# Performance work log

Measured on AMD Instinct MI355X. Metric: run time of the kernel, lower is better.

Reference implementation:

```python
import jax, jax.numpy as jnp
import numpy as np

B, H, M, K = 256, 1024, 20, 20  # batch, hidden, max_ingr, pairing top_k (must be equal: M==K)
VOCAB, INGR_V = 32000, 5000


def setup_inputs() -> dict:
    key = jax.random.key(0)
    ks = jax.random.split(key, 24)
    s = 0.02
    inp = {
        "input_ids": jax.random.randint(ks[0], (1, B), 0, VOCAB),
        "hidden": jax.random.normal(ks[1], (1, B, H), jnp.float32),
        "encoder_outputs": jax.random.normal(ks[2], (M, B, 2 * H), jnp.float32),
        "input_tensor": jax.random.randint(ks[3], (B, M), 0, INGR_V),
        "pairing_ids": jax.random.randint(ks[4], (INGR_V, K), 0, INGR_V),
        # parameters
        "emb_dec": jax.random.normal(ks[5], (VOCAB, H), jnp.float32) * s,
        "enc_emb": jax.random.normal(ks[6], (INGR_V, 2 * H), jnp.float32) * s,
        "Wq_i": jax.random.normal(ks[7], (H, H), jnp.float32) * s,
        "Wk_i": jax.random.normal(ks[8], (2 * H, H), jnp.float32) * s,
        "wa_i": jax.random.normal(ks[9], (H,), jnp.float32) * s,
        "Wq_p": jax.random.normal(ks[10], (H, H), jnp.float32) * s,
        "Wk_p": jax.random.normal(ks[11], (2 * H, H), jnp.float32) * s,
        "wa_p": jax.random.normal(ks[12], (H,), jnp.float32) * s,
        "ba_p": jax.random.normal(ks[13], (), jnp.float32) * s,
        "W_lin": jax.random.normal(ks[14], (3 * H, 2 * H), jnp.float32) * s,
        "b_lin": jnp.zeros((2 * H,), jnp.float32),
        "W_ih": jax.random.normal(ks[15], (3 * H, 2 * H), jnp.float32) * s,
        "W_hh": jax.random.normal(ks[16], (3 * H, H), jnp.float32) * s,
        "b_ih": jnp.zeros((3 * H,), jnp.float32),
        "b_hh": jnp.zeros((3 * H,), jnp.float32),
        "W_out": jax.random.normal(ks[17], (H, VOCAB), jnp.float32) * s,
        "b_out": jnp.zeros((VOCAB,), jnp.float32),
    }
    return inp


def reference(input_ids, hidden, encoder_outputs, input_tensor, pairing_ids,
              emb_dec, enc_emb, Wq_i, Wk_i, wa_i, Wq_p, Wk_p, wa_p, ba_p,
              W_lin, b_lin, W_ih, W_hh, b_ih, b_hh, W_out, b_out):
    h = hidden[0]                              # (B, H)
    emb = jnp.take(emb_dec, input_ids[0], axis=0)  # (B, H)

    # ---- IngrAtt (additive attention over ingredients) ----
    # torch code does a raw .view(B, M, 2H) on a (M, B, 2H) tensor -> plain reshape
    enc = encoder_outputs.reshape(B, M, 2 * H)
    query = h @ Wq_i                           # (B, H)
    key = enc @ Wk_i                           # (B, M, H)
    scores_i = jnp.tanh(query[:, None, :] + key) @ wa_i  # (B, M)
    aw = jax.nn.softmax(scores_i, axis=-1)     # (B, M)

    # ---- retrieval: pick most-attended ingredient, gather its top-k pairings ----
    ingr_arg = jnp.argmax(aw, axis=1)                          # (B,)
    ingr_id = input_tensor[jnp.arange(B), ingr_arg]            # (B,)
    comp_ids = jnp.take(pairing_ids, ingr_id, axis=0)          # (B, K)
    comp_emb = jnp.take(enc_emb, comp_ids, axis=0)             # (B, K, 2H)

    # ---- PairingAtt ----
    q_p = h @ Wq_p                             # (B, H)
    k_p = comp_emb @ Wk_p                      # (B, K, H)
    s_p = jnp.tanh(q_p[:, None, :] + k_p) @ wa_p + ba_p  # (B, K)
    a_p = jax.nn.softmax(s_p, axis=-1)
    attn_scores = a_p * s_p                    # (B, K) softmax-weighted raw scores
    attn_app = jnp.einsum('bk,bkd->bd', attn_scores, comp_emb)  # (B, 2H)

    out_pair = jnp.concatenate([emb, attn_app], axis=-1)  # (B, 3H)
    x = out_pair @ W_lin + b_lin                           # (B, 2H) -> GRU input

    # ---- single GRU step (torch gate ordering r,z,n) ----
    gi = x @ W_ih.T + b_ih
    gh = h @ W_hh.T + b_hh
    i_r, i_z, i_n = jnp.split(gi, 3, axis=-1)
    h_r, h_z, h_n = jnp.split(gh, 3, axis=-1)
    r = jax.nn.sigmoid(i_r + h_r)
    z = jax.nn.sigmoid(i_z + h_z)
    n = jnp.tanh(i_n + r * h_n)
    h_new = (1.0 - z) * n + z * h              # (B, H)

    logits = h_new @ W_out + b_out             # (B, VOCAB)
    return logits
```

## Files before the change

kernel.cpp:

```cpp
#include <hip/hip_runtime.h>
#include <cstdio>


using f32x4   = __attribute__((ext_vector_type(4))) float;
using bf16x8  = __attribute__((ext_vector_type(8))) short;
using ushort8 = __attribute__((ext_vector_type(8))) unsigned short;

__device__ __forceinline__ unsigned short f2bf(float x) {
    unsigned u = __builtin_bit_cast(unsigned, x);
    u += 0x7fffu + ((u >> 16) & 1u);
    return (unsigned short)(u >> 16);
}
__device__ __forceinline__ float bf2f(unsigned short u) {
    return __builtin_bit_cast(float, ((unsigned)u) << 16);
}

__device__ __forceinline__ void gload16(const void* g, void* l) {
    auto gp = (const __attribute__((address_space(1))) void*)g;
    auto lp = (__attribute__((address_space(3))) void*)l;
    __builtin_amdgcn_global_load_lds(gp, lp, 16, 0, 0);
}

__device__ __forceinline__ void transpose_body(
    const float* __restrict__ in, unsigned short* __restrict__ out,
    int R, int C, int r0, int c0)
{
    __shared__ float t[32][129];
    const int tid = threadIdx.x;
    const int lr = tid >> 3;
    const int cc = (tid & 7) * 4;
    #pragma unroll
    for (int i = 0; i < 4; ++i) {
        int r = lr + 32 * i;
        float4 v = *(const float4*)(in + (size_t)(r0 + r) * C + c0 + cc);
        t[cc + 0][r] = v.x; t[cc + 1][r] = v.y;
        t[cc + 2][r] = v.z; t[cc + 3][r] = v.w;
    }
    __syncthreads();
    const int rc = (tid & 15) * 8;
    #pragma unroll
    for (int p = 0; p < 2; ++p) {
        int c = (tid >> 4) + 16 * p;
        const float* src = &t[c][rc];
        ushort8 o;
        #pragma unroll
        for (int j = 0; j < 8; ++j) o[j] = f2bf(src[j]);
        *(ushort8*)(out + (size_t)(c0 + c) * R + r0 + rc) = o;
    }
}

__global__ __launch_bounds__(256) void prep1_kernel(
    const float* __restrict__ hidden, const float* __restrict__ enc_out,
    const float* __restrict__ enc_emb,
    const float* __restrict__ Wq_i, const float* __restrict__ Wq_p,
    const float* __restrict__ Wk_i, const float* __restrict__ Wk_p,
    unsigned short* __restrict__ hb, unsigned short* __restrict__ encb,
    unsigned short* __restrict__ encembb,
    unsigned short* __restrict__ WqiT, unsigned short* __restrict__ WqpT,
    unsigned short* __restrict__ WkiT, unsigned short* __restrict__ WkpT)
{
    const int bid = blockIdx.x;
    if (bid < 20496) {
        int i = bid * 256 + threadIdx.x;
        const float* src; unsigned short* dst; int j;
        if (i < 65536)        { src = hidden;  dst = hb;      j = i; }
        else if (i < 2686976) { src = enc_out; dst = encb;    j = i - 65536; }
        else                  { src = enc_emb; dst = encembb; j = i - 2686976; }
        float4 v = ((const float4*)src)[j];
        ((ushort4*)dst)[j] = make_ushort4(f2bf(v.x), f2bf(v.y), f2bf(v.z), f2bf(v.w));
    } else if (bid < 21008) {
        int local = bid - 20496;
        int bz = local >> 8, rem = local & 255;
        transpose_body(bz ? Wq_p : Wq_i, bz ? WqpT : WqiT,
                       1024, 1024, (rem >> 5) * 128, (rem & 31) * 32);
    } else {
        int local = bid - 21008;
        int bz = local >> 9, rem = local & 511;
        transpose_body(bz ? Wk_p : Wk_i, bz ? WkpT : WkiT,
                       2048, 1024, (rem >> 5) * 128, (rem & 31) * 32);
    }
}

template<int OUTBF, bool HAS_BIAS>
__device__ __forceinline__ void gemm_core(
    const unsigned short* __restrict__ A, const unsigned short* __restrict__ Bt,
    const float* __restrict__ bias, void* __restrict__ Cout, int Ncols,
    int sA, int sB, int kLen, int m0, int n0,
    unsigned short* lA, unsigned short* lB)
{
    const int tid = threadIdx.x;
    const int lane = tid & 63, wave = tid >> 6;
    const int wr = wave >> 1, wc = wave & 1;
    const int srow = tid >> 3, schunk = tid & 7;
    const int lm = lane & 15, lk = (lane >> 4) * 8;

    f32x4 acc[4][4];
    #pragma unroll
    for (int m = 0; m < 4; ++m)
        #pragma unroll
        for (int n = 0; n < 4; ++n) { f32x4 z = {0.f,0.f,0.f,0.f}; acc[m][n] = z; }

    const unsigned short* Ag = A  + (size_t)(m0 + srow) * sA + schunk * 8;
    const unsigned short* Bg = Bt + (size_t)(n0 + srow) * sB + schunk * 8;
    const int nt = kLen >> 6;

    char* lap = (char*)lA + tid * 16;
    char* lbp = (char*)lB + tid * 16;

    for (int t = 0; t < nt; ++t) {
        #pragma unroll
        for (int i = 0; i < 4; ++i) {
            gload16(Ag + (size_t)(32 * i) * sA + t * 64, lap + i * 4096);
            gload16(Bg + (size_t)(32 * i) * sB + t * 64, lbp + i * 4096);
        }
        __syncthreads();
        #pragma unroll
        for (int kk = 0; kk < 2; ++kk) {
            bf16x8 af[4], bv[4];
            #pragma unroll
            for (int m = 0; m < 4; ++m)
                af[m] = *(const bf16x8*)((const char*)lA +
                          (wr * 64 + m * 16 + lm) * 128 + (kk * 32 + lk) * 2);
            #pragma unroll
            for (int n = 0; n < 4; ++n)
                bv[n] = *(const bf16x8*)((const char*)lB +
                          (wc * 64 + n * 16 + lm) * 128 + (kk * 32 + lk) * 2);
            #pragma unroll
            for (int m = 0; m < 4; ++m)
                #pragma unroll
                for (int n = 0; n < 4; ++n)
                    acc[m][n] = __builtin_amdgcn_mfma_f32_16x16x32_bf16(
                        af[m], bv[n], acc[m][n], 0, 0, 0);
        }
        __syncthreads();
    }

    const int rbase = m0 + wr * 64 + (lane >> 4) * 4;
    const int cbase = n0 + wc * 64 + lm;
    #pragma unroll
    for (int m = 0; m < 4; ++m) {
        #pragma unroll
        for (int n = 0; n < 4; ++n) {
            int col = cbase + n * 16;
            float bvv = HAS_BIAS ? bias[col] : 0.0f;
            #pragma unroll
            for (int j = 0; j < 4; ++j) {
                int row = rbase + m * 16 + j;
                float v = acc[m][n][j] + bvv;
                if (OUTBF)
                    ((unsigned short*)Cout)[(size_t)row * Ncols + col] = f2bf(v);
                else
                    ((float*)Cout)[(size_t)row * Ncols + col] = v;
            }
        }
    }
}

#define GEMM_SHARED \
    __shared__ unsigned short lA[8192]; __shared__ unsigned short lB[8192];

__global__ __launch_bounds__(256) void gemm_dual_kernel(
    const unsigned short* A, const unsigned short* B0, const unsigned short* B1,
    float* P0, float* P1)
{
    GEMM_SHARED
    const int g = blockIdx.z >> 2, s = blockIdx.z & 3;
    const unsigned short* Bt = (g ? B1 : B0) + s * 256;
    float* C = (g ? P1 : P0) + (size_t)s * 262144;
    gemm_core<0,false>(A + s * 256, Bt, nullptr, C, 1024, 1024, 1024, 256,
                       blockIdx.y * 128, blockIdx.x * 128, lA, lB);
}

__global__ __launch_bounds__(256) void reduceq_kernel(
    const float* __restrict__ pqQ, const float* __restrict__ pqP,
    float* __restrict__ query, float* __restrict__ qp)
{
    int i = blockIdx.x * 256 + threadIdx.x;
    const float4* p; float4* o; int j;
    if (i < 65536) { p = (const float4*)pqQ; o = (float4*)query; j = i; }
    else           { p = (const float4*)pqP; o = (float4*)qp;    j = i - 65536; }
    float4 a = p[j], b = p[j + 65536], c = p[j + 131072], d = p[j + 196608];
    o[j] = make_float4(a.x + b.x + c.x + d.x, a.y + b.y + c.y + d.y,
                       a.z + b.z + c.z + d.z, a.w + b.w + c.w + d.w);
}

__global__ __launch_bounds__(256) void gemm24_kernel(
    const unsigned short* encembb, const unsigned short* encb,
    const unsigned short* WkpT, const unsigned short* WkiT,
    unsigned short* kpP, unsigned short* keyP, size_t pStride)
{
    GEMM_SHARED
    const int g = blockIdx.z >> 1, h = blockIdx.z & 1;
    const unsigned short* A  = (g ? encb : encembb) + h * 1024;
    const unsigned short* Bt = (g ? WkiT : WkpT)    + h * 1024;
    unsigned short* C = (g ? keyP : kpP) + (size_t)h * pStride;
    gemm_core<1,false>(A, Bt, nullptr, C, 1024, 2048, 2048, 1024,
                       blockIdx.y * 128, blockIdx.x * 128, lA, lB);
}

__global__ __launch_bounds__(256) void gemm5f_kernel(
    const unsigned short* __restrict__ A, const float* __restrict__ Wlin,
    float* __restrict__ P)
{
    __shared__ unsigned short lA[8192];
    __shared__ unsigned short lB[8192];
    const int tid = threadIdx.x;
    const int lane = tid & 63, wave = tid >> 6;
    const int wr = wave >> 1, wc = wave & 1;
    const int m0 = blockIdx.y * 128, n0 = blockIdx.x * 128;
    const int koff = blockIdx.z * 384;
    const int srow = tid >> 3, schunk = tid & 7;
    const int lm = lane & 15, lk = (lane >> 4) * 8;
    const int bcol = tid & 127, bkg = tid >> 7;
    const int bsw  = (bcol & 7) << 4;

    f32x4 acc[4][4];
    #pragma unroll
    for (int m = 0; m < 4; ++m)
        #pragma unroll
        for (int n = 0; n < 4; ++n) { f32x4 z = {0.f,0.f,0.f,0.f}; acc[m][n] = z; }

    const unsigned short* Ag = A + (size_t)(m0 + srow) * 3072 + koff + schunk * 8;
    char* lap = (char*)lA + tid * 16;

    for (int t = 0; t < 6; ++t) {
        #pragma unroll
        for (int i = 0; i < 4; ++i)
            gload16(Ag + (size_t)(32 * i) * 3072 + t * 64, lap + i * 4096);
        #pragma unroll
        for (int hh = 0; hh < 2; ++hh) {
            const int kbase = koff + t * 64 + bkg * 32 + hh * 16;
            ushort8 o0, o1;
            #pragma unroll
            for (int j = 0; j < 8; ++j)
                o0[j] = f2bf(Wlin[(size_t)(kbase + j) * 2048 + n0 + bcol]);
            #pragma unroll
            for (int j = 0; j < 8; ++j)
                o1[j] = f2bf(Wlin[(size_t)(kbase + 8 + j) * 2048 + n0 + bcol]);
            char* base = (char*)lB + bcol * 128;
            *(ushort8*)(base + ((bkg * 64 + hh * 32)      ^ bsw)) = o0;
            *(ushort8*)(base + ((bkg * 64 + hh * 32 + 16) ^ bsw)) = o1;
        }
        __syncthreads();
        #pragma unroll
        for (int kk = 0; kk < 2; ++kk) {
            bf16x8 af[4], bv[4];
            #pragma unroll
            for (int m = 0; m < 4; ++m)
                af[m] = *(const bf16x8*)((const char*)lA +
                          (wr * 64 + m * 16 + lm) * 128 + (kk * 32 + lk) * 2);
            #pragma unroll
            for (int n = 0; n < 4; ++n) {
                int rr = wc * 64 + n * 16 + lm;
                bv[n] = *(const bf16x8*)((const char*)lB +
                          rr * 128 + (((kk * 32 + lk) * 2) ^ ((rr & 7) << 4)));
            }
            #pragma unroll
            for (int m = 0; m < 4; ++m)
                #pragma unroll
                for (int n = 0; n < 4; ++n)
                    acc[m][n] = __builtin_amdgcn_mfma_f32_16x16x32_bf16(
                        af[m], bv[n], acc[m][n], 0, 0, 0);
        }
        __syncthreads();
    }

    float* C = P + (size_t)blockIdx.z * 524288;
    const int rbase = m0 + wr * 64 + (lane >> 4) * 4;
    const int cbase = n0 + wc * 64 + lm;
    #pragma unroll
    for (int m = 0; m < 4; ++m)
        #pragma unroll
        for (int n = 0; n < 4; ++n)
            #pragma unroll
            for (int j = 0; j < 4; ++j)
                C[(size_t)(rbase + m * 16 + j) * 2048 + cbase + n * 16] = acc[m][n][j];
}

__global__ __launch_bounds__(256) void gemm67f_kernel(
    const unsigned short* __restrict__ xb, const unsigned short* __restrict__ hb,
    const float* __restrict__ Wih, const float* __restrict__ Whh,
    float* __restrict__ pg)
{
    __shared__ unsigned short lA[8192];
    __shared__ unsigned short lB[8192];
    const int tid = threadIdx.x;
    const int lane = tid & 63, wave = tid >> 6;
    const int wr = wave >> 1, wc = wave & 1;
    const int g = blockIdx.z >> 2, s = blockIdx.z & 3;
    const unsigned short* A = g ? hb : xb;
    const float* Bf = g ? Whh : Wih;
    const int sA   = g ? 1024 : 2048;
    const int koff = g ? s * 256 : s * 512;
    const int nt   = g ? 4 : 8;
    const int m0 = blockIdx.y * 128, n0 = blockIdx.x * 128;
    const int srow = tid >> 3, schunk = tid & 7;
    const int lm = lane & 15, lk = (lane >> 4) * 8;
    const int bsw = (srow & 7) << 4;

    f32x4 acc[4][4];
    #pragma unroll
    for (int m = 0; m < 4; ++m)
        #pragma unroll
        for (int n = 0; n < 4; ++n) { f32x4 z = {0.f,0.f,0.f,0.f}; acc[m][n] = z; }

    const unsigned short* Ag = A  + (size_t)(m0 + srow) * sA + koff + schunk * 8;
    const float*          Bg = Bf + (size_t)(n0 + srow) * sA + koff + schunk * 8;
    char* lap = (char*)lA + tid * 16;

    for (int t = 0; t < nt; ++t) {
        #pragma unroll
        for (int i = 0; i < 4; ++i)
            gload16(Ag + (size_t)(32 * i) * sA + t * 64, lap + i * 4096);
        #pragma unroll
        for (int i = 0; i < 4; ++i) {
            const float* src = Bg + (size_t)(32 * i) * sA + t * 64;
            float4 v0 = *(const float4*)(src);
            float4 v1 = *(const float4*)(src + 4);
            ushort8 o;
            o[0] = f2bf(v0.x); o[1] = f2bf(v0.y); o[2] = f2bf(v0.z); o[3] = f2bf(v0.w);
            o[4] = f2bf(v1.x); o[5] = f2bf(v1.y); o[6] = f2bf(v1.z); o[7] = f2bf(v1.w);
            *(ushort8*)((char*)lB + (srow + 32 * i) * 128 + ((schunk * 16) ^ bsw)) = o;
        }
        __syncthreads();
        #pragma unroll
        for (int kk = 0; kk < 2; ++kk) {
            bf16x8 af[4], bv[4];
            #pragma unroll
            for (int m = 0; m < 4; ++m)
                af[m] = *(const bf16x8*)((const char*)lA +
                          (wr * 64 + m * 16 + lm) * 128 + (kk * 32 + lk) * 2);
            #pragma unroll
            for (int n = 0; n < 4; ++n) {
                int rr = wc * 64 + n * 16 + lm;
                bv[n] = *(const bf16x8*)((const char*)lB +
                          rr * 128 + (((kk * 32 + lk) * 2) ^ ((rr & 7) << 4)));
            }
            #pragma unroll
            for (int m = 0; m < 4; ++m)
                #pragma unroll
                for (int n = 0; n < 4; ++n)
                    acc[m][n] = __builtin_amdgcn_mfma_f32_16x16x32_bf16(
                        af[m], bv[n], acc[m][n], 0, 0, 0);
        }
        __syncthreads();
    }

    float* C = pg + (size_t)blockIdx.z * 786432;
    const int rbase = m0 + wr * 64 + (lane >> 4) * 4;
    const int cbase = n0 + wc * 64 + lm;
    #pragma unroll
    for (int m = 0; m < 4; ++m)
        #pragma unroll
        for (int n = 0; n < 4; ++n)
            #pragma unroll
            for (int j = 0; j < 4; ++j)
                C[(size_t)(rbase + m * 16 + j) * 3072 + cbase + n * 16] = acc[m][n][j];
}

__global__ __launch_bounds__(256) void gemm8_kernel(
    const unsigned short* __restrict__ A, const float* __restrict__ Wout,
    const float* __restrict__ bias, float* __restrict__ C)
{
    __shared__ unsigned short lA0[16384]; __shared__ unsigned short lA1[16384];
    __shared__ unsigned short lB0[4096];  __shared__ unsigned short lB1[4096];
    const int tid  = threadIdx.x;
    const int lane = tid & 63, wave = tid >> 6;
    const int n0 = blockIdx.x * 64;
    const int lm = lane & 15, lk = (lane >> 4) * 8;
    const int srow = tid >> 3, schunk = tid & 7;
    const int bcol = tid & 63, bkg = tid >> 6;
    const int bsw  = (bcol & 7) << 4;

    f32x4 acc[4][4];
    #pragma unroll
    for (int m = 0; m < 4; ++m)
        #pragma unroll
        for (int n = 0; n < 4; ++n) { f32x4 z = {0.f,0.f,0.f,0.f}; acc[m][n] = z; }

    const unsigned short* Ag = A + (size_t)srow * 1024 + schunk * 8;

    auto stageA = [&](unsigned short* la_, int t) {
        char* la = (char*)la_ + tid * 16;
        #pragma unroll
        for (int i = 0; i < 8; ++i)
            gload16(Ag + (size_t)(32 * i) * 1024 + t * 64, la + i * 4096);
    };
    float bv_[16];
    auto loadB = [&](int t) {
        const float* src = Wout + (size_t)(t * 64 + bkg * 16) * 32000 + n0 + bcol;
        #pragma unroll
        for (int j = 0; j < 16; ++j) bv_[j] = src[(size_t)j * 32000];
    };
    auto writeB = [&](unsigned short* lb_) {
        ushort8 o0, o1;
        #pragma unroll
        for (int j = 0; j < 8; ++j) { o0[j] = f2bf(bv_[j]); o1[j] = f2bf(bv_[j + 8]); }
        char* base = (char*)lb_ + bcol * 128;
        *(ushort8*)(base + ((bkg * 32)      ^ bsw)) = o0;
        *(ushort8*)(base + ((bkg * 32 + 16) ^ bsw)) = o1;
    };
    auto compute = [&](const unsigned short* la_, const unsigned short* lb_) {
        #pragma unroll
        for (int kk = 0; kk < 2; ++kk) {
            bf16x8 af[4], bv[4];
            #pragma unroll
            for (int m = 0; m < 4; ++m)
                af[m] = *(const bf16x8*)((const char*)la_ +
                          (wave * 64 + m * 16 + lm) * 128 + (kk * 32 + lk) * 2);
            #pragma unroll
            for (int n = 0; n < 4; ++n) {
                int rr = n * 16 + lm;
                bv[n] = *(const bf16x8*)((const char*)lb_ +
                          rr * 128 + (((kk * 32 + lk) * 2) ^ ((rr & 7) << 4)));
            }
            #pragma unroll
            for (int m = 0; m < 4; ++m)
                #pragma unroll
                for (int n = 0; n < 4; ++n)
                    acc[m][n] = __builtin_amdgcn_mfma_f32_16x16x32_bf16(
                        af[m], bv[n], acc[m][n], 0, 0, 0);
        }
    };

    stageA(lA0, 0); loadB(0); writeB(lB0);
    __syncthreads();
    const int nt = 16;
    for (int t = 0; t < nt; t += 2) {
        if (t + 1 < nt) { stageA(lA1, t + 1); loadB(t + 1); }
        compute(lA0, lB0);
        if (t + 1 < nt) writeB(lB1);
        __syncthreads();
        if (t + 1 < nt) {
            if (t + 2 < nt) { stageA(lA0, t + 2); loadB(t + 2); }
            compute(lA1, lB1);
            if (t + 2 < nt) writeB(lB0);
            __syncthreads();
        }
    }

    const int rbase = wave * 64 + (lane >> 4) * 4;
    const int cbase = n0 + lm;
    #pragma unroll
    for (int m = 0; m < 4; ++m) {
        #pragma unroll
        for (int n = 0; n < 4; ++n) {
            int col = cbase + n * 16;
            float bvv = bias[col];
            #pragma unroll
            for (int j = 0; j < 4; ++j)
                C[(size_t)(rbase + m * 16 + j) * 32000 + col] = acc[m][n][j] + bvv;
        }
    }
}

__global__ __launch_bounds__(256) void attn_scores2_kernel(
    const float* __restrict__ q, const unsigned short* __restrict__ kP,
    size_t kStride, const float* __restrict__ wa, float* __restrict__ scores)
{
    const int bm = blockIdx.x;
    const int b  = bm / 20;
    const int tid = threadIdx.x;
    float4 qv  = ((const float4*)(q + (size_t)b * 1024))[tid];
    ushort4 k0 = ((const ushort4*)(kP + (size_t)bm * 1024))[tid];
    ushort4 k1 = ((const ushort4*)(kP + kStride + (size_t)bm * 1024))[tid];
    float4 wv  = ((const float4*)wa)[tid];
    float p = tanhf(qv.x + bf2f(k0.x) + bf2f(k1.x)) * wv.x
            + tanhf(qv.y + bf2f(k0.y) + bf2f(k1.y)) * wv.y
            + tanhf(qv.z + bf2f(k0.z) + bf2f(k1.z)) * wv.z
            + tanhf(qv.w + bf2f(k0.w) + bf2f(k1.w)) * wv.w;
    #pragma unroll
    for (int off = 32; off > 0; off >>= 1) p += __shfl_down(p, off);
    __shared__ float sp[4];
    if ((tid & 63) == 0) sp[tid >> 6] = p;
    __syncthreads();
    if (tid == 0) scores[bm] = sp[0] + sp[1] + sp[2] + sp[3];
}

__device__ __forceinline__ int argmax_ing(
    const float* __restrict__ sc_i, const int* __restrict__ input_tensor, int b)
{
    float best = sc_i[b * 20]; int bi = 0;
    #pragma unroll
    for (int m = 1; m < 20; ++m) {
        float v = sc_i[b * 20 + m];
        if (v > best) { best = v; bi = m; }
    }
    return input_tensor[b * 20 + bi];
}

__global__ __launch_bounds__(256) void attn_scores_gather2_kernel(
    const float* __restrict__ q, const unsigned short* __restrict__ kP,
    size_t kStride, const float* __restrict__ wa, const float* __restrict__ ba,
    const float* __restrict__ sc_i, const int* __restrict__ input_tensor,
    const int* __restrict__ pairing_ids, float* __restrict__ scores)
{
    const int bm = blockIdx.x;
    const int b  = bm / 20;
    const int kk = bm - b * 20;
    const int tid = threadIdx.x;
    const int ing = argmax_ing(sc_i, input_tensor, b);
    const int cid = pairing_ids[ing * 20 + kk];
    float4 qv  = ((const float4*)(q + (size_t)b * 1024))[tid];
    ushort4 k0 = ((const ushort4*)(kP + (size_t)cid * 1024))[tid];
    ushort4 k1 = ((const ushort4*)(kP + kStride + (size_t)cid * 1024))[tid];
    float4 wv  = ((const float4*)wa)[tid];
    float p = tanhf(qv.x + bf2f(k0.x) + bf2f(k1.x)) * wv.x
            + tanhf(qv.y + bf2f(k0.y) + bf2f(k1.y)) * wv.y
            + tanhf(qv.z + bf2f(k0.z) + bf2f(k1.z)) * wv.z
            + tanhf(qv.w + bf2f(k0.w) + bf2f(k1.w)) * wv.w;
    #pragma unroll
    for (int off = 32; off > 0; off >>= 1) p += __shfl_down(p, off);
    __shared__ float sp[4];
    if ((tid & 63) == 0) sp[tid >> 6] = p;
    __syncthreads();
    if (tid == 0) scores[bm] = sp[0] + sp[1] + sp[2] + sp[3] + ba[0];
}

__global__ __launch_bounds__(256) void out_pair_kernel(
    const float* __restrict__ s_p, const float* __restrict__ enc_emb,
    const float* __restrict__ sc_i, const int* __restrict__ input_tensor,
    const int* __restrict__ pairing_ids,
    const float* __restrict__ emb_dec, const int* __restrict__ input_ids,
    unsigned short* __restrict__ out_pairb)
{
    const int b = blockIdx.x / 6, seg = blockIdx.x % 6;
    const int tid = threadIdx.x;
    const int d = seg * 512 + tid * 2;
    ushort2 o;
    if (seg < 2) {
        float2 v = *(const float2*)(emb_dec + (size_t)input_ids[b] * 1024 + d);
        o.x = f2bf(v.x); o.y = f2bf(v.y);
    } else {
        const int ing = argmax_ing(sc_i, input_tensor, b);
        __shared__ float s_raw[20];
        if (tid < 20) s_raw[tid] = s_p[b * 20 + tid];
        __syncthreads();
        float mx = -1e30f;
        #pragma unroll
        for (int m = 0; m < 20; ++m) mx = fmaxf(mx, s_raw[m]);
        float den = 0.f; float w[20];
        #pragma unroll
        for (int m = 0; m < 20; ++m) { w[m] = expf(s_raw[m] - mx); den += w[m]; }
        const float inv = 1.f / den;
        const int dd = d - 1024;
        float a0 = 0.f, a1 = 0.f;
        #pragma unroll
        for (int k = 0; k < 20; ++k) {
            const int cid = pairing_ids[ing * 20 + k];
            float2 v = *(const float2*)(enc_emb + (size_t)cid * 2048 + dd);
            float a = w[k] * inv * s_raw[k];
            a0 += a * v.x; a1 += a * v.y;
        }
        o.x = f2bf(a0); o.y = f2bf(a1);
    }
    *(ushort2*)(out_pairb + (size_t)b * 3072 + d) = o;
}

__global__ __launch_bounds__(256) void reduce5_kernel(
    const float* __restrict__ P, const float* __restrict__ bias,
    unsigned short* __restrict__ xb)
{
    int i = blockIdx.x * 256 + threadIdx.x;
    const float4* p = (const float4*)P;
    float4 bb = ((const float4*)bias)[i & 511];
    float s0 = bb.x, s1 = bb.y, s2 = bb.z, s3 = bb.w;
    #pragma unroll
    for (int s = 0; s < 8; ++s) {
        float4 v = p[i + s * 131072];
        s0 += v.x; s1 += v.y; s2 += v.z; s3 += v.w;
    }
    ((ushort4*)xb)[i] = make_ushort4(f2bf(s0), f2bf(s1), f2bf(s2), f2bf(s3));
}

__global__ __launch_bounds__(256) void gru_kernel(
    const float* __restrict__ pg, const float* __restrict__ b_ih,
    const float* __restrict__ b_hh, const float* __restrict__ h,
    unsigned short* __restrict__ hnewb)
{
    int idx = blockIdx.x * 256 + threadIdx.x;
    int b = idx >> 10, j = idx & 1023;
    float ir = b_ih[j], iz = b_ih[1024 + j], in_ = b_ih[2048 + j];
    float hr = b_hh[j], hz = b_hh[1024 + j], hn  = b_hh[2048 + j];
    #pragma unroll
    for (int s = 0; s < 4; ++s) {
        const float* gi = pg + (size_t)s * 786432 + (size_t)b * 3072;
        ir  += gi[j]; iz += gi[1024 + j]; in_ += gi[2048 + j];
        const float* gh = pg + (size_t)(4 + s) * 786432 + (size_t)b * 3072;
        hr  += gh[j]; hz += gh[1024 + j]; hn  += gh[2048 + j];
    }
    float r = 1.f / (1.f + expf(-(ir + hr)));
    float z = 1.f / (1.f + expf(-(iz + hz)));
    float n = tanhf(in_ + r * hn);
    hnewb[idx] = f2bf((1.f - z) * n + z * h[idx]);
}

extern "C" void kernel_launch(void* const* d_in, const int* in_sizes, int n_in,
                              void* d_out, int out_size, void* d_ws, size_t ws_size,
                              hipStream_t stream)
{
    const int*   input_ids    = (const int*)  d_in[0];
    const float* hidden       = (const float*)d_in[1];
    const float* enc_out      = (const float*)d_in[2];
    const int*   input_tensor = (const int*)  d_in[3];
    const int*   pairing_ids  = (const int*)  d_in[4];
    const float* emb_dec      = (const float*)d_in[5];
    const float* enc_emb      = (const float*)d_in[6];
    const float* Wq_i  = (const float*)d_in[7];
    const float* Wk_i  = (const float*)d_in[8];
    const float* wa_i  = (const float*)d_in[9];
    const float* Wq_p  = (const float*)d_in[10];
    const float* Wk_p  = (const float*)d_in[11];
    const float* wa_p  = (const float*)d_in[12];
    const float* ba_p  = (const float*)d_in[13];
    const float* W_lin = (const float*)d_in[14];
    const float* b_lin = (const float*)d_in[15];
    const float* W_ih  = (const float*)d_in[16];
    const float* W_hh  = (const float*)d_in[17];
    const float* b_ih  = (const float*)d_in[18];
    const float* b_hh  = (const float*)d_in[19];
    const float* W_out = (const float*)d_in[20];
    const float* b_out = (const float*)d_in[21];

    constexpr size_t OFF_HB    = 0;
    constexpr size_t OFF_HNEW  = 524288;
    constexpr size_t OFF_WQI   = 1048576;
    constexpr size_t OFF_WQP   = 3145728;
    constexpr size_t OFF_WKI   = 5242880;
    constexpr size_t OFF_WKP   = 9437184;
    constexpr size_t OFF_ENC   = 13631488;
    constexpr size_t OFF_SLOT1 = 34603008;
    constexpr size_t OFF_SLOT2 = 55574528;
    constexpr size_t OFF_QUERY = 76546048;
    constexpr size_t OFF_QP    = 77594624;
    constexpr size_t OFF_SCI   = 78643200;
    constexpr size_t OFF_SCP   = 78667776;
    constexpr size_t OFF_PGI   = 1048576;
    constexpr size_t NEED      = 79167488;
    if (ws_size < NEED) {
        fprintf(stderr, "kernel_launch: ws_size %zu < needed %zu\n", ws_size, NEED);
        return;
    }
    char* ws = (char*)d_ws;
    unsigned short* hb     = (unsigned short*)(ws + OFF_HB);
    unsigned short* hnewb  = (unsigned short*)(ws + OFF_HNEW);
    unsigned short* WqiT   = (unsigned short*)(ws + OFF_WQI);
    unsigned short* WqpT   = (unsigned short*)(ws + OFF_WQP);
    unsigned short* WkiT   = (unsigned short*)(ws + OFF_WKI);
    unsigned short* WkpT   = (unsigned short*)(ws + OFF_WKP);
    unsigned short* encb   = (unsigned short*)(ws + OFF_ENC);
    float*          pqQ    = (float*)         (ws + OFF_SLOT1);
    float*          pqP    = (float*)         (ws + OFF_SLOT1 + 4194304);
    unsigned short* kpP    = (unsigned short*)(ws + OFF_SLOT1);
    unsigned short* encembb= (unsigned short*)(ws + OFF_SLOT2);
    unsigned short* outp   = (unsigned short*)(ws + OFF_SLOT1);
    float*          pG5    = (float*)         (ws + OFF_SLOT1 + 1572864);
    unsigned short* xb     = (unsigned short*)(ws + OFF_SLOT1 + 18350080);
    float*          query  = (float*)         (ws + OFF_QUERY);
    float*          qp     = (float*)         (ws + OFF_QP);
    float*          sc_i   = (float*)         (ws + OFF_SCI);
    float*          sc_p   = (float*)         (ws + OFF_SCP);
    float*          pgi    = (float*)         (ws + OFF_PGI);
    unsigned short* keyP   = (unsigned short*)d_out;

    constexpr size_t KP_STRIDE = 5120 * 1024;

    prep1_kernel<<<22032, 256, 0, stream>>>(hidden, enc_out, enc_emb,
                                            Wq_i, Wq_p, Wk_i, Wk_p,
                                            hb, encb, encembb,
                                            WqiT, WqpT, WkiT, WkpT);

    gemm_dual_kernel<<<dim3(8, 2, 8), 256, 0, stream>>>(hb, WqiT, WqpT, pqQ, pqP);
    reduceq_kernel<<<512, 256, 0, stream>>>(pqQ, pqP, query, qp);

    gemm24_kernel<<<dim3(8, 40, 4), 256, 0, stream>>>(encembb, encb, WkpT, WkiT,
                                                      kpP, keyP, KP_STRIDE);

    attn_scores2_kernel<<<5120, 256, 0, stream>>>(query, keyP, KP_STRIDE, wa_i, sc_i);
    attn_scores_gather2_kernel<<<5120, 256, 0, stream>>>(qp, kpP, KP_STRIDE, wa_p, ba_p,
                                                         sc_i, input_tensor, pairing_ids, sc_p);

    out_pair_kernel<<<1536, 256, 0, stream>>>(sc_p, enc_emb, sc_i, input_tensor,
                                              pairing_ids, emb_dec, input_ids, outp);

    gemm5f_kernel<<<dim3(16, 2, 8), 256, 0, stream>>>(outp, W_lin, pG5);
    reduce5_kernel<<<512, 256, 0, stream>>>(pG5, b_lin, xb);

    gemm67f_kernel<<<dim3(24, 2, 8), 256, 0, stream>>>(xb, hb, W_ih, W_hh, pgi);

    gru_kernel<<<1024, 256, 0, stream>>>(pgi, b_ih, b_hh, hidden, hnewb);

    gemm8_kernel<<<500, 256, 0, stream>>>(hnewb, W_out, b_out, (float*)d_out);
}
```

Before: 230.6 us.

## Merge query GEMM into key GEMM launch and fold split-K reduce into score kernels

The small split-K query projection GEMMs (Wq_i, Wq_p) now run as extra blocks inside the large key-projection GEMM launch, removing one launch and letting both run concurrently. The separate reduceq kernel is dropped; each attention-score block instead sums the four split-K partials itself. The partials move into the unused tail of the output buffer so they no longer collide with the kpP slot now written in the same launch. Score blocks now make four q reads instead of one, which are repeated across the 20 blocks per batch row.

```diff
diff --git a/kernel.cpp b/kernel.cpp
--- a/kernel.cpp
+++ b/kernel.cpp
@@ -159,43 +159,149 @@
 #define GEMM_SHARED \
     __shared__ unsigned short lA[8192]; __shared__ unsigned short lB[8192];
 
-__global__ __launch_bounds__(256) void gemm_dual_kernel(
-    const unsigned short* A, const unsigned short* B0, const unsigned short* B1,
-    float* P0, float* P1)
-{
-    GEMM_SHARED
-    const int g = blockIdx.z >> 2, s = blockIdx.z & 3;
-    const unsigned short* Bt = (g ? B1 : B0) + s * 256;
-    float* C = (g ? P1 : P0) + (size_t)s * 262144;
-    gemm_core<0,false>(A + s * 256, Bt, nullptr, C, 1024, 1024, 1024, 256,
-                       blockIdx.y * 128, blockIdx.x * 128, lA, lB);
-}
-
-__global__ __launch_bounds__(256) void reduceq_kernel(
-    const float* __restrict__ pqQ, const float* __restrict__ pqP,
-    float* __restrict__ query, float* __restrict__ qp)
-{
-    int i = blockIdx.x * 256 + threadIdx.x;
-    const float4* p; float4* o; int j;
-    if (i < 65536) { p = (const float4*)pqQ; o = (float4*)query; j = i; }
-    else           { p = (const float4*)pqP; o = (float4*)qp;    j = i - 65536; }
-    float4 a = p[j], b = p[j + 65536], c = p[j + 131072], d = p[j + 196608];
-    o[j] = make_float4(a.x + b.x + c.x + d.x, a.y + b.y + c.y + d.y,
-                       a.z + b.z + c.z + d.z, a.w + b.w + c.w + d.w);
-}
-
-__global__ __launch_bounds__(256) void gemm24_kernel(
+__global__ __launch_bounds__(256) void gemm24d_kernel(
+    const unsigned short* hb,
+    const unsigned short* WqiT, const unsigned short* WqpT,
+    float* pqQ, float* pqP,
     const unsigned short* encembb, const unsigned short* encb,
     const unsigned short* WkpT, const unsigned short* WkiT,
     unsigned short* kpP, unsigned short* keyP, size_t pStride)
 {
     GEMM_SHARED
-    const int g = blockIdx.z >> 1, h = blockIdx.z & 1;
-    const unsigned short* A  = (g ? encb : encembb) + h * 1024;
-    const unsigned short* Bt = (g ? WkiT : WkpT)    + h * 1024;
-    unsigned short* C = (g ? keyP : kpP) + (size_t)h * pStride;
-    gemm_core<1,false>(A, Bt, nullptr, C, 1024, 2048, 2048, 1024,
-                       blockIdx.y * 128, blockIdx.x * 128, lA, lB);
+    const int id = blockIdx.x;
+    if (id < 128) {
+        const int bx = id & 7, by = (id >> 3) & 1, zz = id >> 4;
+        const int g = zz >> 2, s = zz & 3;
+        const unsigned short* Bt = (g ? WqpT : WqiT) + s * 256;
+        float* C = (g ? pqP : pqQ) + (size_t)s * 262144;
+        gemm_core<0,false>(hb + s * 256, Bt, nullptr, C, 1024, 1024, 1024, 256,
+                           by * 128, bx * 128, lA, lB);
+    } else {
+        const int id2 = id - 128;
+        const int bx  = id2 & 7;
+        const int rem = id2 >> 3;
+        const int by  = rem % 40;
+        const int zz  = rem / 40;
+        const int g = zz >> 1, h = zz & 1;
+        const unsigned short* A  = (g ? encb : encembb) + h * 1024;
+        const unsigned short* Bt = (g ? WkiT : WkpT)    + h * 1024;
+        unsigned short* C = (g ? keyP : kpP) + (size_t)h * pStride;
+        gemm_core<1,false>(A, Bt, nullptr, C, 1024, 2048, 2048, 1024,
+                           by * 128, bx * 128, lA, lB);
+    }
+}
+
+__global__ __launch_bounds__(256) void attn_scores2q_kernel(
+    const float* __restrict__ pqQ, const unsigned short* __restrict__ kP,
+    size_t kStride, const float* __restrict__ wa, float* __restrict__ scores)
+{
+    const int bm = blockIdx.x;
+    const int b  = bm / 20;
+    const int tid = threadIdx.x;
+    float4 qa = ((const float4*)(pqQ + (size_t)b * 1024))[tid];
+    float4 qb = ((const float4*)(pqQ + 262144 + (size_t)b * 1024))[tid];
+    float4 qc = ((const float4*)(pqQ + 524288 + (size_t)b * 1024))[tid];
+    float4 qd = ((const float4*)(pqQ + 786432 + (size_t)b * 1024))[tid];
+    float4 qv = make_float4(qa.x + qb.x + qc.x + qd.x, qa.y + qb.y + qc.y + qd.y,
+                            qa.z + qb.z + qc.z + qd.z, qa.w + qb.w + qc.w + qd.w);
+    ushort4 k0 = ((const ushort4*)(kP + (size_t)bm * 1024))[tid];
+    ushort4 k1 = ((const ushort4*)(kP + kStride + (size_t)bm * 1024))[tid];
+    float4 wv  = ((const float4*)wa)[tid];
+    float p = tanhf(qv.x + bf2f(k0.x) + bf2f(k1.x)) * wv.x
+            + tanhf(qv.y + bf2f(k0.y) + bf2f(k1.y)) * wv.y
+            + tanhf(qv.z + bf2f(k0.z) + bf2f(k1.z)) * wv.z
+            + tanhf(qv.w + bf2f(k0.w) + bf2f(k1.w)) * wv.w;
+    #pragma unroll
+    for (int off = 32; off > 0; off >>= 1) p += __shfl_down(p, off);
+    __shared__ float sp[4];
+    if ((tid & 63) == 0) sp[tid >> 6] = p;
+    __syncthreads();
+    if (tid == 0) scores[bm] = sp[0] + sp[1] + sp[2] + sp[3];
+}
+
+__device__ __forceinline__ int argmax_ing(
+    const float* __restrict__ sc_i, const int* __restrict__ input_tensor, int b)
+{
+    float best = sc_i[b * 20]; int bi = 0;
+    #pragma unroll
+    for (int m = 1; m < 20; ++m) {
+        float v = sc_i[b * 20 + m];
+        if (v > best) { best = v; bi = m; }
+    }
+    return input_tensor[b * 20 + bi];
+}
+
+__global__ __launch_bounds__(256) void attn_scores_gather2q_kernel(
+    const float* __restrict__ pqP, const unsigned short* __restrict__ kP,
+    size_t kStride, const float* __restrict__ wa, const float* __restrict__ ba,
+    const float* __restrict__ sc_i, const int* __restrict__ input_tensor,
+    const int* __restrict__ pairing_ids, float* __restrict__ scores)
+{
+    const int bm = blockIdx.x;
+    const int b  = bm / 20;
+    const int kk = bm - b * 20;
+    const int tid = threadIdx.x;
+    const int ing = argmax_ing(sc_i, input_tensor, b);
+    const int cid = pairing_ids[ing * 20 + kk];
+    float4 qa = ((const float4*)(pqP + (size_t)b * 1024))[tid];
+    float4 qb = ((const float4*)(pqP + 262144 + (size_t)b * 1024))[tid];
+    float4 qc = ((const float4*)(pqP + 524288 + (size_t)b * 1024))[tid];
+    float4 qd = ((const float4*)(pqP + 786432 + (size_t)b * 1024))[tid];
+    float4 qv = make_float4(qa.x + qb.x + qc.x + qd.x, qa.y + qb.y + qc.y + qd.y,
+                            qa.z + qb.z + qc.z + qd.z, qa.w + qb.w + qc.w + qd.w);
+    ushort4 k0 = ((const ushort4*)(kP + (size_t)cid * 1024))[tid];
+    ushort4 k1 = ((const ushort4*)(kP + kStride + (size_t)cid * 1024))[tid];
+    float4 wv  = ((const float4*)wa)[tid];
+    float p = tanhf(qv.x + bf2f(k0.x) + bf2f(k1.x)) * wv.x
+            + tanhf(qv.y + bf2f(k0.y) + bf2f(k1.y)) * wv.y
+            + tanhf(qv.z + bf2f(k0.z) + bf2f(k1.z)) * wv.z
+            + tanhf(qv.w + bf2f(k0.w) + bf2f(k1.w)) * wv.w;
+    #pragma unroll
+    for (int off = 32; off > 0; off >>= 1) p += __shfl_down(p, off);
+    __shared__ float sp[4];
+    if ((tid & 63) == 0) sp[tid >> 6] = p;
+    __syncthreads();
+    if (tid == 0) scores[bm] = sp[0] + sp[1] + sp[2] + sp[3] + ba[0];
+}
+
+__global__ __launch_bounds__(256) void out_pair_kernel(
+    const float* __restrict__ s_p, const float* __restrict__ enc_emb,
+    const float* __restrict__ sc_i, const int* __restrict__ input_tensor,
+    const int* __restrict__ pairing_ids,
+    const float* __restrict__ emb_dec, const int* __restrict__ input_ids,
+    unsigned short* __restrict__ out_pairb)
+{
+    const int b = blockIdx.x / 6, seg = blockIdx.x % 6;
+    const int tid = threadIdx.x;
+    const int d = seg * 512 + tid * 2;
+    ushort2 o;
+    if (seg < 2) {
+        float2 v = *(const float2*)(emb_dec + (size_t)input_ids[b] * 1024 + d);
+        o.x = f2bf(v.x); o.y = f2bf(v.y);
+    } else {
+        const int ing = argmax_ing(sc_i, input_tensor, b);
+        __shared__ float s_raw[20];
+        if (tid < 20) s_raw[tid] = s_p[b * 20 + tid];
+        __syncthreads();
+        float mx = -1e30f;
+        #pragma unroll
+        for (int m = 0; m < 20; ++m) mx = fmaxf(mx, s_raw[m]);
+        float den = 0.f; float w[20];
+        #pragma unroll
+        for (int m = 0; m < 20; ++m) { w[m] = expf(s_raw[m] - mx); den += w[m]; }
+        const float inv = 1.f / den;
+        const int dd = d - 1024;
+        float a0 = 0.f, a1 = 0.f;
+        #pragma unroll
+        for (int k = 0; k < 20; ++k) {
+            const int cid = pairing_ids[ing * 20 + k];
+            float2 v = *(const float2*)(enc_emb + (size_t)cid * 2048 + dd);
+            float a = w[k] * inv * s_raw[k];
+            a0 += a * v.x; a1 += a * v.y;
+        }
+        o.x = f2bf(a0); o.y = f2bf(a1);
+    }
+    *(ushort2*)(out_pairb + (size_t)b * 3072 + d) = o;
 }
 
 __global__ __launch_bounds__(256) void gemm5f_kernel(
@@ -452,109 +558,6 @@
                 C[(size_t)(rbase + m * 16 + j) * 32000 + col] = acc[m][n][j] + bvv;
         }
     }
-}
-
-__global__ __launch_bounds__(256) void attn_scores2_kernel(
-    const float* __restrict__ q, const unsigned short* __restrict__ kP,
-    size_t kStride, const float* __restrict__ wa, float* __restrict__ scores)
-{
-    const int bm = blockIdx.x;
-    const int b  = bm / 20;
-    const int tid = threadIdx.x;
-    float4 qv  = ((const float4*)(q + (size_t)b * 1024))[tid];
-    ushort4 k0 = ((const ushort4*)(kP + (size_t)bm * 1024))[tid];
-    ushort4 k1 = ((const ushort4*)(kP + kStride + (size_t)bm * 1024))[tid];
-    float4 wv  = ((const float4*)wa)[tid];
-    float p = tanhf(qv.x + bf2f(k0.x) + bf2f(k1.x)) * wv.x
-            + tanhf(qv.y + bf2f(k0.y) + bf2f(k1.y)) * wv.y
-            + tanhf(qv.z + bf2f(k0.z) + bf2f(k1.z)) * wv.z
-            + tanhf(qv.w + bf2f(k0.w) + bf2f(k1.w)) * wv.w;
-    #pragma unroll
-    for (int off = 32; off > 0; off >>= 1) p += __shfl_down(p, off);
-    __shared__ float sp[4];
-    if ((tid & 63) == 0) sp[tid >> 6] = p;
-    __syncthreads();
-    if (tid == 0) scores[bm] = sp[0] + sp[1] + sp[2] + sp[3];
-}
-
-__device__ __forceinline__ int argmax_ing(
-    const float* __restrict__ sc_i, const int* __restrict__ input_tensor, int b)
-{
-    float best = sc_i[b * 20]; int bi = 0;
-    #pragma unroll
-    for (int m = 1; m < 20; ++m) {
-        float v = sc_i[b * 20 + m];
-        if (v > best) { best = v; bi = m; }
-    }
-    return input_tensor[b * 20 + bi];
-}
-
-__global__ __launch_bounds__(256) void attn_scores_gather2_kernel(
-    const float* __restrict__ q, const unsigned short* __restrict__ kP,
-    size_t kStride, const float* __restrict__ wa, const float* __restrict__ ba,
-    const float* __restrict__ sc_i, const int* __restrict__ input_tensor,
-    const int* __restrict__ pairing_ids, float* __restrict__ scores)
-{
-    const int bm = blockIdx.x;
-    const int b  = bm / 20;
-    const int kk = bm - b * 20;
-    const int tid = threadIdx.x;
-    const int ing = argmax_ing(sc_i, input_tensor, b);
-    const int cid = pairing_ids[ing * 20 + kk];
-    float4 qv  = ((const float4*)(q + (size_t)b * 1024))[tid];
-    ushort4 k0 = ((const ushort4*)(kP + (size_t)cid * 1024))[tid];
-    ushort4 k1 = ((const ushort4*)(kP + kStride + (size_t)cid * 1024))[tid];
-    float4 wv  = ((const float4*)wa)[tid];
-    float p = tanhf(qv.x + bf2f(k0.x) + bf2f(k1.x)) * wv.x
-            + tanhf(qv.y + bf2f(k0.y) + bf2f(k1.y)) * wv.y
-            + tanhf(qv.z + bf2f(k0.z) + bf2f(k1.z)) * wv.z
-            + tanhf(qv.w + bf2f(k0.w) + bf2f(k1.w)) * wv.w;
-    #pragma unroll
-    for (int off = 32; off > 0; off >>= 1) p += __shfl_down(p, off);
-    __shared__ float sp[4];
-    if ((tid & 63) == 0) sp[tid >> 6] = p;
-    __syncthreads();
-    if (tid == 0) scores[bm] = sp[0] + sp[1] + sp[2] + sp[3] + ba[0];
-}
-
-__global__ __launch_bounds__(256) void out_pair_kernel(
-    const float* __restrict__ s_p, const float* __restrict__ enc_emb,
-    const float* __restrict__ sc_i, const int* __restrict__ input_tensor,
-    const int* __restrict__ pairing_ids,
-    const float* __restrict__ emb_dec, const int* __restrict__ input_ids,
-    unsigned short* __restrict__ out_pairb)
-{
-    const int b = blockIdx.x / 6, seg = blockIdx.x % 6;
-    const int tid = threadIdx.x;
-    const int d = seg * 512 + tid * 2;
-    ushort2 o;
-    if (seg < 2) {
-        float2 v = *(const float2*)(emb_dec + (size_t)input_ids[b] * 1024 + d);
-        o.x = f2bf(v.x); o.y = f2bf(v.y);
-    } else {
-        const int ing = argmax_ing(sc_i, input_tensor, b);
-        __shared__ float s_raw[20];
-        if (tid < 20) s_raw[tid] = s_p[b * 20 + tid];
-        __syncthreads();
-        float mx = -1e30f;
-        #pragma unroll
-        for (int m = 0; m < 20; ++m) mx = fmaxf(mx, s_raw[m]);
-        float den = 0.f; float w[20];
-        #pragma unroll
-        for (int m = 0; m < 20; ++m) { w[m] = expf(s_raw[m] - mx); den += w[m]; }
-        const float inv = 1.f / den;
-        const int dd = d - 1024;
-        float a0 = 0.f, a1 = 0.f;
-        #pragma unroll
-        for (int k = 0; k < 20; ++k) {
-            const int cid = pairing_ids[ing * 20 + k];
-            float2 v = *(const float2*)(enc_emb + (size_t)cid * 2048 + dd);
-            float a = w[k] * inv * s_raw[k];
-            a0 += a * v.x; a1 += a * v.y;
-        }
-        o.x = f2bf(a0); o.y = f2bf(a1);
-    }
-    *(ushort2*)(out_pairb + (size_t)b * 3072 + d) = o;
 }
 
 __global__ __launch_bounds__(256) void reduce5_kernel(
@@ -631,8 +634,6 @@
     constexpr size_t OFF_ENC   = 13631488;
     constexpr size_t OFF_SLOT1 = 34603008;
     constexpr size_t OFF_SLOT2 = 55574528;
-    constexpr size_t OFF_QUERY = 76546048;
-    constexpr size_t OFF_QP    = 77594624;
     constexpr size_t OFF_SCI   = 78643200;
     constexpr size_t OFF_SCP   = 78667776;
     constexpr size_t OFF_PGI   = 1048576;
@@ -649,19 +650,17 @@
     unsigned short* WkiT   = (unsigned short*)(ws + OFF_WKI);
     unsigned short* WkpT   = (unsigned short*)(ws + OFF_WKP);
     unsigned short* encb   = (unsigned short*)(ws + OFF_ENC);
-    float*          pqQ    = (float*)         (ws + OFF_SLOT1);
-    float*          pqP    = (float*)         (ws + OFF_SLOT1 + 4194304);
     unsigned short* kpP    = (unsigned short*)(ws + OFF_SLOT1);
     unsigned short* encembb= (unsigned short*)(ws + OFF_SLOT2);
     unsigned short* outp   = (unsigned short*)(ws + OFF_SLOT1);
     float*          pG5    = (float*)         (ws + OFF_SLOT1 + 1572864);
     unsigned short* xb     = (unsigned short*)(ws + OFF_SLOT1 + 18350080);
-    float*          query  = (float*)         (ws + OFF_QUERY);
-    float*          qp     = (float*)         (ws + OFF_QP);
     float*          sc_i   = (float*)         (ws + OFF_SCI);
     float*          sc_p   = (float*)         (ws + OFF_SCP);
     float*          pgi    = (float*)         (ws + OFF_PGI);
     unsigned short* keyP   = (unsigned short*)d_out;
+    float*          pqQ    = (float*)((char*)d_out + 20971520);
+    float*          pqP    = (float*)((char*)d_out + 20971520 + 4194304);
 
     constexpr size_t KP_STRIDE = 5120 * 1024;
 
@@ -670,15 +669,13 @@
                                             hb, encb, encembb,
                                             WqiT, WqpT, WkiT, WkpT);
 
-    gemm_dual_kernel<<<dim3(8, 2, 8), 256, 0, stream>>>(hb, WqiT, WqpT, pqQ, pqP);
-    reduceq_kernel<<<512, 256, 0, stream>>>(pqQ, pqP, query, qp);
-
-    gemm24_kernel<<<dim3(8, 40, 4), 256, 0, stream>>>(encembb, encb, WkpT, WkiT,
-                                                      kpP, keyP, KP_STRIDE);
-
-    attn_scores2_kernel<<<5120, 256, 0, stream>>>(query, keyP, KP_STRIDE, wa_i, sc_i);
-    attn_scores_gather2_kernel<<<5120, 256, 0, stream>>>(qp, kpP, KP_STRIDE, wa_p, ba_p,
-                                                         sc_i, input_tensor, pairing_ids, sc_p);
+    gemm24d_kernel<<<1408, 256, 0, stream>>>(hb, WqiT, WqpT, pqQ, pqP,
+                                             encembb, encb, WkpT, WkiT,
+                                             kpP, keyP, KP_STRIDE);
+
+    attn_scores2q_kernel<<<5120, 256, 0, stream>>>(pqQ, keyP, KP_STRIDE, wa_i, sc_i);
+    attn_scores_gather2q_kernel<<<5120, 256, 0, stream>>>(pqP, kpP, KP_STRIDE, wa_p, ba_p,
+                                                          sc_i, input_tensor, pairing_ids, sc_p);
 
     out_pair_kernel<<<1536, 256, 0, stream>>>(sc_p, enc_emb, sc_i, input_tensor,
                                               pairing_ids, emb_dec, input_ids, outp);
```

Measured after the change: 232.8 us. Within noise of the previous version (+0.9%).
